# Kernel tuning notes

Hardware: AMD Instinct MI355X
Metric: run time of the kernel (lower is better)

## Reference

```python
import jax, jax.numpy as jnp
import numpy as np

D_MODEL = 2048
N_HEADS = 16
D_HEAD = D_MODEL // N_HEADS
BATCH = 2
SEQ = 2048
NEG = -1e9


def setup_inputs() -> dict:
    key = jax.random.key(0)
    ks = jax.random.split(key, 6)
    s = 1.0 / np.sqrt(D_MODEL)
    x = jax.random.normal(ks[0], (BATCH, SEQ, D_MODEL), dtype=jnp.float32)
    # additive causal mask: 0 on/below diagonal, -1e9 above
    causal = jnp.where(jnp.tril(jnp.ones((SEQ, SEQ), dtype=bool)), 0.0, NEG).astype(jnp.float32)
    return {
        "x": x,
        "mask": causal,
        "Wq": jax.random.normal(ks[1], (D_MODEL, D_MODEL), dtype=jnp.float32) * s,
        "bq": jnp.zeros((D_MODEL,), dtype=jnp.float32),
        "Wk": jax.random.normal(ks[2], (D_MODEL, D_MODEL), dtype=jnp.float32) * s,
        "bk": jnp.zeros((D_MODEL,), dtype=jnp.float32),
        "Wv": jax.random.normal(ks[3], (D_MODEL, D_MODEL), dtype=jnp.float32) * s,
        "bv": jnp.zeros((D_MODEL,), dtype=jnp.float32),
        "Wo": jax.random.normal(ks[4], (D_MODEL, D_MODEL), dtype=jnp.float32) * s,
        "bo": jnp.zeros((D_MODEL,), dtype=jnp.float32),
    }


def reference(x, mask, Wq, bq, Wk, bk, Wv, bv, Wo, bo):
    B, S, _ = x.shape
    scale = 1.0 / np.sqrt(D_HEAD).astype(np.float32)
    # projections -> (B, H, S, Dh)
    def split_heads(t):
        return t.reshape(B, S, N_HEADS, D_HEAD).transpose(0, 2, 1, 3)
    q = split_heads(x @ Wq + bq)
    k = split_heads(x @ Wk + bk)
    v = split_heads(x @ Wv + bv)
    scores = jnp.einsum("bhqd,bhkd->bhqk", q, k) * scale + mask  # (B,H,S,S)
    weights = jax.nn.softmax(scores, axis=-1)
    attn = jnp.einsum("bhqk,bhkd->bhqd", weights, v)
    attn = attn.transpose(0, 2, 1, 3).reshape(B, S, D_MODEL)
    return attn @ Wo + bo
```

## Files before the change

### kernel.cpp

```cpp
#include <hip/hip_runtime.h>
#include <hip/hip_bf16.h>
#include <math.h>

typedef __bf16 bf16;
typedef __attribute__((ext_vector_type(4))) __bf16 bf16x4;
typedef __attribute__((ext_vector_type(8))) __bf16 bf16x8;
typedef __attribute__((ext_vector_type(4))) float f32x4;
typedef __attribute__((ext_vector_type(4))) int i32x4;

#define DEV __device__ __forceinline__
#define FENCE asm volatile("" ::: "memory")

static constexpr int S_LEN = 2048;
static constexpr int DM = 2048;
static constexpr int NB = 2;
static constexpr int NH = 16;
static constexpr int DH = 128;
static constexpr long MROWS = (long)NB * S_LEN;

static constexpr float QSCALE = 0.12751744836522312f;
static constexpr float M0 = 11.0f;


__global__ void k_cast_bf16(const float* __restrict__ in, bf16* __restrict__ out, long n8) {
  long i = (long)blockIdx.x * blockDim.x + threadIdx.x;
  long stride = (long)gridDim.x * blockDim.x;
  for (; i < n8; i += stride) {
    const float4* p = (const float4*)(in + i * 8);
    float4 a = p[0], b = p[1];
    bf16x8 v;
    v[0] = (bf16)a.x; v[1] = (bf16)a.y; v[2] = (bf16)a.z; v[3] = (bf16)a.w;
    v[4] = (bf16)b.x; v[5] = (bf16)b.y; v[6] = (bf16)b.z; v[7] = (bf16)b.w;
    *(bf16x8*)(out + i * 8) = v;
  }
}

__global__ void k_transpose_w(const float* __restrict__ in, bf16* __restrict__ out) {
  __shared__ float t[32][33];
  int bx = blockIdx.x * 32, by = blockIdx.y * 32;
  int tx = threadIdx.x, ty = threadIdx.y;
#pragma unroll
  for (int i = 0; i < 32; i += 8)
    t[ty + i][tx] = in[(long)(by + ty + i) * DM + bx + tx];
  __syncthreads();
#pragma unroll
  for (int i = 0; i < 32; i += 8)
    out[(long)(bx + ty + i) * DM + by + tx] = (bf16)t[tx][ty + i];
}

__global__ void k_transpose_w3(const float* __restrict__ w0, const float* __restrict__ w1,
                               const float* __restrict__ w2, bf16* __restrict__ out) {
  __shared__ float t[32][33];
  int z = blockIdx.z;
  const float* in = (z == 0) ? w0 : (z == 1) ? w1 : w2;
  bf16* o = out + (long)z * DM * DM;
  int bx = blockIdx.x * 32, by = blockIdx.y * 32;
  int tx = threadIdx.x, ty = threadIdx.y;
#pragma unroll
  for (int i = 0; i < 32; i += 8)
    t[ty + i][tx] = in[(long)(by + ty + i) * DM + bx + tx];
  __syncthreads();
#pragma unroll
  for (int i = 0; i < 32; i += 8)
    o[(long)(bx + ty + i) * DM + by + tx] = (bf16)t[tx][ty + i];
}


DEV void stg_round(const bf16* __restrict__ g, long gstride, bf16* l, int tid, int c) {
  int o = c * 8192 + tid * 16;
  int row = o >> 7;
  int blk = (o >> 4) & 7;
  const bf16* src = g + (long)row * gstride + ((blk ^ (row & 7)) << 3);
  char* dst = (char*)l + (o & ~1023);
  __builtin_amdgcn_global_load_lds(
      (const __attribute__((address_space(1))) void*)src,
      (__attribute__((address_space(3))) void*)dst, 16, 0, 0);
}

template<int ROWB>
DEV void stage16k(const bf16* __restrict__ g, long gstride, bf16* l, int tid) {
#pragma unroll
  for (int c = 0; c < 4; ++c) {
    int o = c * 4096 + tid * 16;
    int row = o / ROWB;
    int blk = (o & (ROWB - 1)) >> 4;
    int blkg = blk ^ (row & 7);
    const bf16* src = g + (long)row * gstride + (blkg << 3);
    char* dst = (char*)l + (o & ~1023);
    __builtin_amdgcn_global_load_lds(
        (const __attribute__((address_space(1))) void*)src,
        (__attribute__((address_space(3))) void*)dst, 16, 0, 0);
  }
}

DEV void stage_k(const bf16* __restrict__ g, bf16* l, int tid) {
#pragma unroll
  for (int c = 0; c < 4; ++c) {
    int o = c * 4096 + tid * 16;
    int row = o >> 8;
    int blk = (o >> 4) & 15;
    int blkg = blk ^ (row & 7);
    int prow = (row & 3) | (((row >> 2) & 3) << 3) | (((row >> 5) & 1) << 2) |
               (((row >> 4) & 1) << 5);
    const bf16* src = g + (long)prow * DM + (blkg << 3);
    char* dst = (char*)l + (o & ~1023);
    __builtin_amdgcn_global_load_lds(
        (const __attribute__((address_space(1))) void*)src,
        (__attribute__((address_space(3))) void*)dst, 16, 0, 0);
  }
}

template<int ROWB>
DEV bf16x8 read_frag(const bf16* l, int row, int blk) {
  int blks = blk ^ (row & 7);
  return *(const bf16x8*)((const char*)l + row * ROWB + (blks << 4));
}


__global__ __launch_bounds__(512) void k_gemm_qkv(const bf16* __restrict__ A,
                                                  const bf16* __restrict__ WTqkv,
                                                  const float* __restrict__ bq,
                                                  const float* __restrict__ bk,
                                                  const float* __restrict__ bv,
                                                  bf16* __restrict__ Qb,
                                                  bf16* __restrict__ Kb,
                                                  bf16* __restrict__ Vt) {
  extern __shared__ char smem[];
  int tid = threadIdx.x;
  int w = tid >> 6, lane = tid & 63;
  int wm = w >> 2, wn = w & 3;
  int g = lane >> 4, c16 = lane & 15;
  long row0 = (long)blockIdx.y * 256;
  long col0 = (long)blockIdx.x * 256;
  int proj = (int)(col0 >> 11);
  int lcol0 = (int)(col0 & 2047);
  const float* bias = (proj == 0) ? bq : (proj == 1) ? bk : bv;
  const bf16* gA = A + row0 * 2048;
  const bf16* gB = WTqkv + col0 * 2048;

  f32x4 acc[8][4] = {};

#define BA(i) ((bf16*)(smem + (i) * 65536))
#define BB(i) ((bf16*)(smem + (i) * 65536 + 32768))

#pragma unroll
  for (int c = 0; c < 4; ++c) stg_round(gA, 2048, BA(0), tid, c);
#pragma unroll
  for (int c = 0; c < 4; ++c) stg_round(gB, 2048, BB(0), tid, c);
  asm volatile("s_waitcnt vmcnt(0)" ::: "memory");
  __builtin_amdgcn_s_barrier();
  FENCE;

#pragma unroll 1
  for (int t = 0; t < 32; ++t) {
    int cur = t & 1, nxt = cur ^ 1;
    bf16* cA = BA(cur);
    bf16* cB = BB(cur);
    bool st = (t + 1) < 32;
    if (st) {
      const bf16* gA2 = gA + (t + 1) * 64;
      const bf16* gB2 = gB + (t + 1) * 64;
#pragma unroll
      for (int c = 0; c < 4; ++c) stg_round(gA2, 2048, BA(nxt), tid, c);
#pragma unroll
      for (int c = 0; c < 4; ++c) stg_round(gB2, 2048, BB(nxt), tid, c);
    }
    bf16x8 af[4], bj[4];
#pragma unroll
    for (int ks = 0; ks < 2; ++ks) {
#pragma unroll
      for (int j = 0; j < 4; ++j)
        bj[j] = read_frag<128>(cB, wn * 64 + j * 16 + c16, ks * 4 + g);
#pragma unroll
      for (int rh = 0; rh < 2; ++rh) {
#pragma unroll
        for (int i = 0; i < 4; ++i)
          af[i] = read_frag<128>(cA, wm * 128 + rh * 64 + i * 16 + c16, ks * 4 + g);
        __builtin_amdgcn_s_setprio(1);
#pragma unroll
        for (int i = 0; i < 4; ++i)
#pragma unroll
          for (int j = 0; j < 4; ++j)
            acc[rh * 4 + i][j] =
                __builtin_amdgcn_mfma_f32_16x16x32_bf16(af[i], bj[j], acc[rh * 4 + i][j], 0, 0, 0);
        __builtin_amdgcn_s_setprio(0);
      }
    }
    if (st) {
      asm volatile("s_waitcnt vmcnt(0)" ::: "memory");
      FENCE; __builtin_amdgcn_s_barrier(); FENCE;
    }
  }

#pragma unroll
  for (int i = 0; i < 8; ++i) {
    long grow = row0 + wm * 128 + i * 16 + (g << 2);
#pragma unroll
    for (int j = 0; j < 4; ++j) {
      int lcol = lcol0 + wn * 64 + j * 16 + c16;
      float bv_ = bias[lcol];
      if (proj == 2) {
        int b = (int)(grow >> 11), s = (int)(grow & 2047);
        int h = lcol >> 7, d = lcol & 127;
        bf16x4 pk;
#pragma unroll
        for (int r = 0; r < 4; ++r) pk[r] = (bf16)(acc[i][j][r] + bv_);
        *(bf16x4*)(Vt + ((long)((b << 4) | h) * 128 + d) * 2048 + s) = pk;
      } else {
        bf16* dst = (proj == 0) ? Qb : Kb;
        float cs = (proj == 0) ? QSCALE : 1.0f;
#pragma unroll
        for (int r = 0; r < 4; ++r)
          dst[(grow + r) * 2048 + lcol] = (bf16)((acc[i][j][r] + bv_) * cs);
      }
    }
  }
#undef BA
#undef BB
}


DEV void gemm_loop(const bf16* __restrict__ gA, const bf16* __restrict__ gB,
                   char* smem, int tid, int wm, int wn, int g, int c16,
                   f32x4 (&acc)[4][4]) {
#define BUFA(i) ((bf16*)(smem + (i) * 49152))
#define BUFB(i) ((bf16*)(smem + (i) * 49152 + 32768))

#pragma unroll
  for (int t0 = 0; t0 < 2; ++t0) {
#pragma unroll
    for (int c = 0; c < 4; ++c) stg_round(gA + t0 * 64, 2048, BUFA(t0), tid, c);
#pragma unroll
    for (int c = 0; c < 2; ++c) stg_round(gB + t0 * 64, 2048, BUFB(t0), tid, c);
  }
  asm volatile("s_waitcnt vmcnt(6)" ::: "memory");
  __builtin_amdgcn_s_barrier();
  FENCE;

#pragma unroll 1
  for (int t = 0; t < 32; ++t) {
    bf16* cA = BUFA(t % 3);
    bf16* cB = BUFB(t % 3);
    bf16* nA = BUFA((t + 2) % 3);
    bf16* nB = BUFB((t + 2) % 3);
    const bf16* gA2 = gA + (t + 2) * 64;
    const bf16* gB2 = gB + (t + 2) * 64;
    bool st = (t + 2) < 32;
    bf16x8 af[4], bj[4];

    if (st) { stg_round(gA2, 2048, nA, tid, 0); stg_round(gA2, 2048, nA, tid, 1);
              stg_round(gA2, 2048, nA, tid, 2); }
#pragma unroll
    for (int i = 0; i < 4; ++i) af[i] = read_frag<128>(cA, wm * 64 + i * 16 + c16, g);
#pragma unroll
    for (int j = 0; j < 4; ++j) bj[j] = read_frag<128>(cB, wn * 64 + j * 16 + c16, g);
    __builtin_amdgcn_s_setprio(1);
#pragma unroll
    for (int i = 0; i < 4; ++i)
#pragma unroll
      for (int j = 0; j < 4; ++j)
        acc[i][j] = __builtin_amdgcn_mfma_f32_16x16x32_bf16(af[i], bj[j], acc[i][j], 0, 0, 0);
    __builtin_amdgcn_s_setprio(0);
    FENCE; __builtin_amdgcn_s_barrier(); FENCE;

    if (st) { stg_round(gA2, 2048, nA, tid, 3);
              stg_round(gB2, 2048, nB, tid, 0); stg_round(gB2, 2048, nB, tid, 1); }
#pragma unroll
    for (int i = 0; i < 4; ++i) af[i] = read_frag<128>(cA, wm * 64 + i * 16 + c16, 4 + g);
#pragma unroll
    for (int j = 0; j < 4; ++j) bj[j] = read_frag<128>(cB, wn * 64 + j * 16 + c16, 4 + g);
    __builtin_amdgcn_s_setprio(1);
#pragma unroll
    for (int i = 0; i < 4; ++i)
#pragma unroll
      for (int j = 0; j < 4; ++j)
        acc[i][j] = __builtin_amdgcn_mfma_f32_16x16x32_bf16(af[i], bj[j], acc[i][j], 0, 0, 0);
    __builtin_amdgcn_s_setprio(0);
    if (t + 2 < 32) {
      asm volatile("s_waitcnt vmcnt(6)" ::: "memory");
    } else if (t + 1 < 32) {
      asm volatile("s_waitcnt vmcnt(0)" ::: "memory");
    }
    FENCE; __builtin_amdgcn_s_barrier(); FENCE;
  }
#undef BUFA
#undef BUFB
}

__global__ __launch_bounds__(512) void k_gemm_o(const bf16* __restrict__ A,
                                                const bf16* __restrict__ BT,
                                                const float* __restrict__ bias,
                                                float* __restrict__ C) {
  extern __shared__ char smem[];
  int tid = threadIdx.x;
  int w = tid >> 6, lane = tid & 63;
  int wm = w >> 1, wn = w & 1;
  int g = lane >> 4, c16 = lane & 15;
  long row0 = (long)blockIdx.y * 256, col0 = (long)blockIdx.x * 128;

  f32x4 acc[4][4] = {};
  gemm_loop(A + row0 * 2048, BT + col0 * 2048, smem, tid, wm, wn, g, c16, acc);

#pragma unroll
  for (int i = 0; i < 4; ++i) {
    long grow = row0 + wm * 64 + i * 16 + (g << 2);
#pragma unroll
    for (int j = 0; j < 4; ++j) {
      long gcol = col0 + wn * 64 + j * 16 + c16;
      float bv = bias[gcol];
#pragma unroll
      for (int r = 0; r < 4; ++r)
        C[(grow + r) * 2048 + gcol] = acc[i][j][r] + bv;
    }
  }
}


__global__ __launch_bounds__(256, 2) void k_attn(const bf16* __restrict__ Q,
                                                 const bf16* __restrict__ Kt,
                                                 const bf16* __restrict__ Vt,
                                                 bf16* __restrict__ O,
                                                 bf16* __restrict__ part,
                                                 float* __restrict__ lsums) {
  __shared__ __align__(16) bf16 sK[2][64 * 128];
  __shared__ __align__(16) bf16 sV[2][128 * 64];

  int tid = threadIdx.x;
  int bid = blockIdx.x;
  int bh = bid & 31;
  int pr = (bid >> 5) & 7;
  int role = bid >> 8;
  int b = bh >> 4, h = bh & 15;
  int w = tid >> 6, lane = tid & 63;
  int g = lane >> 4, c16 = lane & 15;
  int t = bh * 8 + pr;

  const bf16* Qh = Q + (long)b * S_LEN * DM + h * DH;
  const bf16* Kh = Kt + (long)b * S_LEN * DM + h * DH;
  const bf16* Vh = Vt + (long)bh * DH * S_LEN;

#pragma unroll 1
  for (int seg = 0; seg < 2; ++seg) {
    int qt, k0, k1, partial;
    if (role == 0) {
      if (seg == 0) { qt = pr;      k0 = 0;           k1 = 2 * pr + 2;  partial = 0; }
      else          { qt = 15 - pr; k0 = 0;           k1 = 15 - 2 * pr; partial = 1; }
    } else {
      if (seg == 1) break;
      qt = 15 - pr; k0 = 15 - 2 * pr; k1 = 32 - 2 * pr; partial = 2;
    }

    int q0 = qt * 128;
    int qb = q0 + w * 32;

    bf16x8 qa[2][4];
#pragma unroll
    for (int u = 0; u < 2; ++u)
#pragma unroll
      for (int ks = 0; ks < 4; ++ks)
        qa[u][ks] = *(const bf16x8*)(Qh + (long)(qb + 16 * u + c16) * DM + (ks * 4 + g) * 8);

    stage_k(Kh + (long)k0 * 64 * DM, sK[0], tid);
    stage16k<128>(Vh + k0 * 64, S_LEN, sV[0], tid);

    float lsum[2] = {0.f, 0.f};
    f32x4 od[2][8] = {};

#pragma unroll 1
    for (int kt = k0; kt < k1; ++kt) {
      int cur = (kt - k0) & 1;
      if (kt + 1 < k1) {
        stage_k(Kh + (long)(kt + 1) * 64 * DM, sK[cur ^ 1], tid);
        stage16k<128>(Vh + (kt + 1) * 64, S_LEN, sV[cur ^ 1], tid);
        asm volatile("s_waitcnt vmcnt(8)" ::: "memory");
      } else {
        asm volatile("s_waitcnt vmcnt(0)" ::: "memory");
      }
      __builtin_amdgcn_s_barrier();
      FENCE;

      int kv0 = kt * 64;
      if (kv0 <= qb + 31) {
        f32x4 sf[2][4] = {};
        __builtin_amdgcn_s_setprio(1);
#pragma unroll
        for (int n = 0; n < 4; ++n)
#pragma unroll
          for (int ks = 0; ks < 4; ++ks) {
            bf16x8 kf = read_frag<256>(sK[cur], n * 16 + c16, ks * 4 + g);
            sf[0][n] = __builtin_amdgcn_mfma_f32_16x16x32_bf16(kf, qa[0][ks], sf[0][n], 0, 0, 0);
            sf[1][n] = __builtin_amdgcn_mfma_f32_16x16x32_bf16(kf, qa[1][ks], sf[1][n], 0, 0, 0);
          }
        __builtin_amdgcn_s_setprio(0);

        bool emask = (kv0 + 63 > qb);
        bf16x8 pa[2][2];
#pragma unroll
        for (int u = 0; u < 2; ++u) {
          unsigned pw[8];
#pragma unroll
          for (int n = 0; n < 4; ++n) {
            float pv4[4];
#pragma unroll
            for (int r = 0; r < 4; ++r) {
              float sc = sf[u][n][r];
              if (emask) {
                int kv = kv0 + ((n & 1) << 5) + (g << 3) + ((n >> 1) << 2) + r;
                int qg = qb + 16 * u + c16;
                sc = (kv > qg) ? -INFINITY : sc;
              }
              float pv = exp2f(sc - M0);
              pv4[r] = pv;
              lsum[u] += pv;
            }
            asm("v_cvt_pk_bf16_f32 %0, %1, %2" : "=v"(pw[2 * n]) : "v"(pv4[0]), "v"(pv4[1]));
            asm("v_cvt_pk_bf16_f32 %0, %1, %2" : "=v"(pw[2 * n + 1]) : "v"(pv4[2]), "v"(pv4[3]));
          }
          i32x4 t0 = {(int)pw[0], (int)pw[1], (int)pw[4], (int)pw[5]};
          i32x4 t1 = {(int)pw[2], (int)pw[3], (int)pw[6], (int)pw[7]};
          pa[u][0] = __builtin_bit_cast(bf16x8, t0);
          pa[u][1] = __builtin_bit_cast(bf16x8, t1);
        }

        __builtin_amdgcn_s_setprio(1);
#pragma unroll
        for (int j = 0; j < 8; ++j)
#pragma unroll
          for (int ks = 0; ks < 2; ++ks) {
            bf16x8 vf = read_frag<128>(sV[cur], j * 16 + c16, ks * 4 + g);
            od[0][j] = __builtin_amdgcn_mfma_f32_16x16x32_bf16(pa[0][ks], vf, od[0][j], 0, 0, 0);
            od[1][j] = __builtin_amdgcn_mfma_f32_16x16x32_bf16(pa[1][ks], vf, od[1][j], 0, 0, 0);
          }
        __builtin_amdgcn_s_setprio(0);
      }
      FENCE;
      __builtin_amdgcn_s_barrier();
    }

#pragma unroll
    for (int u = 0; u < 2; ++u) {
      lsum[u] += __shfl_xor(lsum[u], 16);
      lsum[u] += __shfl_xor(lsum[u], 32);
    }

    if (partial == 0) {
      const long ob = ((long)(b * S_LEN + qb)) * DM + h * DH + c16;
#pragma unroll
      for (int u = 0; u < 2; ++u)
#pragma unroll
        for (int r = 0; r < 4; ++r) {
          float inv = 1.0f / __shfl(lsum[u], 4 * g + r);
#pragma unroll
          for (int j = 0; j < 8; ++j)
            O[ob + (long)(16 * u + 4 * g + r) * DM + j * 16] = (bf16)(od[u][j][r] * inv);
        }
    } else {
      bf16* PP = part + ((long)((partial == 2 ? 256 : 0) + t)) * 16384;
      float* LP = lsums + (partial == 2 ? 256 * 128 : 0) + t * 128;
#pragma unroll
      for (int u = 0; u < 2; ++u) {
        if (g == 0) LP[32 * w + 16 * u + c16] = lsum[u];
#pragma unroll
        for (int r = 0; r < 4; ++r) {
          int row = 32 * w + 16 * u + 4 * g + r;
#pragma unroll
          for (int j = 0; j < 8; ++j)
            PP[row * 128 + 16 * j + c16] = (bf16)od[u][j][r];
        }
      }
    }
  }
}

__global__ __launch_bounds__(256) void k_merge(const bf16* __restrict__ part,
                                               const float* __restrict__ lsums,
                                               bf16* __restrict__ A2) {
  int t = blockIdx.x;
  int bh = t >> 3, pr = t & 7;
  int b = bh >> 4, h = bh & 15;
  int qt = 15 - pr;
  int tid = threadIdx.x;
  int q = tid >> 1, d0 = (tid & 1) * 64;
  float inv = 1.0f / (lsums[t * 128 + q] + lsums[256 * 128 + t * 128 + q]);
  const bf16* pA = part + (long)t * 16384 + q * 128 + d0;
  const bf16* pB = part + (long)(256 + t) * 16384 + q * 128 + d0;
  bf16* out = A2 + ((long)(b * S_LEN + qt * 128 + q)) * DM + h * DH + d0;
#pragma unroll
  for (int j = 0; j < 8; ++j) {
    bf16x8 a = *(const bf16x8*)(pA + j * 8);
    bf16x8 bb = *(const bf16x8*)(pB + j * 8);
    bf16x8 o;
#pragma unroll
    for (int r = 0; r < 8; ++r) o[r] = (bf16)(((float)a[r] + (float)bb[r]) * inv);
    *(bf16x8*)(out + j * 8) = o;
  }
}


extern "C" void kernel_launch(void* const* d_in, const int* in_sizes, int n_in,
                              void* d_out, int out_size, void* d_ws, size_t ws_size,
                              hipStream_t stream) {
  (void)in_sizes; (void)n_in; (void)out_size; (void)ws_size;
  const float* x  = (const float*)d_in[0];
  const float* Wq = (const float*)d_in[2];
  const float* bq = (const float*)d_in[3];
  const float* Wk = (const float*)d_in[4];
  const float* bk = (const float*)d_in[5];
  const float* Wv = (const float*)d_in[6];
  const float* bv = (const float*)d_in[7];
  const float* Wo = (const float*)d_in[8];
  const float* bo = (const float*)d_in[9];
  float* out = (float*)d_out;

  bf16* Xb = (bf16*)d_ws;
  bf16* WT = Xb + MROWS * DM;
  bf16* Qb = WT + (long)DM * DM;
  bf16* Kb = Qb + MROWS * DM;
  bf16* Vt = Kb + MROWS * DM;
  bf16* A2 = Xb;

  bf16* WTqkv = (bf16*)d_out;
  bf16* part = (bf16*)d_out;
  float* lsums = (float*)((bf16*)d_out + 2L * 256 * 16384);

  static const int QKV_LDS = 2 * 65536;
  static const int O_LDS = 3 * 49152;
  hipFuncSetAttribute((const void*)k_gemm_qkv, hipFuncAttributeMaxDynamicSharedMemorySize, QKV_LDS);
  hipFuncSetAttribute((const void*)k_gemm_o, hipFuncAttributeMaxDynamicSharedMemorySize, O_LDS);

  dim3 tb32(32, 8);
  dim3 gW(64, 64);

  k_cast_bf16<<<2048, 256, 0, stream>>>(x, Xb, MROWS * DM / 8);
  k_transpose_w3<<<dim3(64, 64, 3), tb32, 0, stream>>>(Wq, Wk, Wv, WTqkv);

  k_gemm_qkv<<<dim3(24, 16), 512, QKV_LDS, stream>>>(Xb, WTqkv, bq, bk, bv, Qb, Kb, Vt);

  k_attn<<<512, 256, 0, stream>>>(Qb, Kb, Vt, A2, part, lsums);
  k_merge<<<256, 256, 0, stream>>>(part, lsums, A2);

  k_transpose_w<<<gW, tb32, 0, stream>>>(Wo, WT);
  k_gemm_o<<<dim3(16, 16), 512, O_LDS, stream>>>(A2, WT, bo, out);
}
```

Before: 254.8 us.

## Widen QKV GEMM tile to 256x384 with 12 waves and 256 blocks

The QKV projection GEMM now uses 768-thread blocks (12 waves in a 2x6 layout) over 256x384 output tiles, which cuts the grid from 384 to 256 blocks, one per CU on a 256-CU part, and removes the partial second wave. Staging is rewritten as a per-wave chunk loop that loads the A and wider B tiles into a larger 160KB double-buffered LDS region. Because a tile can now span two projections, the epilogue picks the projection and bias per column. The cost is more LDS per block and higher register pressure at 768 threads, since each wave still holds 8x4 accumulators.

```diff
diff --git a/kernel.cpp b/kernel.cpp
--- a/kernel.cpp
+++ b/kernel.cpp
@@ -117,7 +117,7 @@
 }
 
 
-__global__ __launch_bounds__(512) void k_gemm_qkv(const bf16* __restrict__ A,
+__global__ __launch_bounds__(768) void k_gemm_qkv(const bf16* __restrict__ A,
                                                   const bf16* __restrict__ WTqkv,
                                                   const float* __restrict__ bq,
                                                   const float* __restrict__ bk,
@@ -128,25 +128,40 @@
   extern __shared__ char smem[];
   int tid = threadIdx.x;
   int w = tid >> 6, lane = tid & 63;
-  int wm = w >> 2, wn = w & 3;
+  int wm = w / 6, wn = w % 6;
   int g = lane >> 4, c16 = lane & 15;
   long row0 = (long)blockIdx.y * 256;
-  long col0 = (long)blockIdx.x * 256;
-  int proj = (int)(col0 >> 11);
-  int lcol0 = (int)(col0 & 2047);
-  const float* bias = (proj == 0) ? bq : (proj == 1) ? bk : bv;
+  long col0 = (long)blockIdx.x * 384;
   const bf16* gA = A + row0 * 2048;
   const bf16* gB = WTqkv + col0 * 2048;
 
   f32x4 acc[8][4] = {};
 
-#define BA(i) ((bf16*)(smem + (i) * 65536))
-#define BB(i) ((bf16*)(smem + (i) * 65536 + 32768))
-
-#pragma unroll
-  for (int c = 0; c < 4; ++c) stg_round(gA, 2048, BA(0), tid, c);
-#pragma unroll
-  for (int c = 0; c < 4; ++c) stg_round(gB, 2048, BB(0), tid, c);
+#define BA(i) ((bf16*)(smem + (i) * 81920))
+#define BB(i) ((bf16*)(smem + (i) * 81920 + 32768))
+
+#define STAGE_TILE(aP, bP, lA, lB)                                                          \
+  do {                                                                                      \
+    for (int ch = w; ch < 80; ch += 12) {                                                   \
+      if (ch < 32) {                                                                        \
+        int o = ch * 1024 + lane * 16;                                                      \
+        int row = o >> 7, blk = (o >> 4) & 7;                                               \
+        __builtin_amdgcn_global_load_lds(                                                   \
+            (const __attribute__((address_space(1))) void*)((aP) + (long)row * 2048 +      \
+                                                            ((blk ^ (row & 7)) << 3)),      \
+            (__attribute__((address_space(3))) void*)((char*)(lA) + (o & ~1023)), 16, 0, 0);\
+      } else {                                                                              \
+        int o = (ch - 32) * 1024 + lane * 16;                                               \
+        int row = o >> 7, blk = (o >> 4) & 7;                                               \
+        __builtin_amdgcn_global_load_lds(                                                   \
+            (const __attribute__((address_space(1))) void*)((bP) + (long)row * 2048 +      \
+                                                            ((blk ^ (row & 7)) << 3)),      \
+            (__attribute__((address_space(3))) void*)((char*)(lB) + (o & ~1023)), 16, 0, 0);\
+      }                                                                                     \
+    }                                                                                       \
+  } while (0)
+
+  STAGE_TILE(gA, gB, BA(0), BB(0));
   asm volatile("s_waitcnt vmcnt(0)" ::: "memory");
   __builtin_amdgcn_s_barrier();
   FENCE;
@@ -157,14 +172,8 @@
     bf16* cA = BA(cur);
     bf16* cB = BB(cur);
     bool st = (t + 1) < 32;
-    if (st) {
-      const bf16* gA2 = gA + (t + 1) * 64;
-      const bf16* gB2 = gB + (t + 1) * 64;
-#pragma unroll
-      for (int c = 0; c < 4; ++c) stg_round(gA2, 2048, BA(nxt), tid, c);
-#pragma unroll
-      for (int c = 0; c < 4; ++c) stg_round(gB2, 2048, BB(nxt), tid, c);
-    }
+    if (st) STAGE_TILE(gA + (t + 1) * 64, gB + (t + 1) * 64, BA(nxt), BB(nxt));
+
     bf16x8 af[4], bj[4];
 #pragma unroll
     for (int ks = 0; ks < 2; ++ks) {
@@ -197,11 +206,13 @@
     long grow = row0 + wm * 128 + i * 16 + (g << 2);
 #pragma unroll
     for (int j = 0; j < 4; ++j) {
-      int lcol = lcol0 + wn * 64 + j * 16 + c16;
-      float bv_ = bias[lcol];
+      int gcol = (int)col0 + wn * 64 + j * 16 + c16;
+      int proj = gcol >> 11;
+      int cc = gcol & 2047;
+      float bv_ = ((proj == 0) ? bq : (proj == 1) ? bk : bv)[cc];
       if (proj == 2) {
         int b = (int)(grow >> 11), s = (int)(grow & 2047);
-        int h = lcol >> 7, d = lcol & 127;
+        int h = cc >> 7, d = cc & 127;
         bf16x4 pk;
 #pragma unroll
         for (int r = 0; r < 4; ++r) pk[r] = (bf16)(acc[i][j][r] + bv_);
@@ -211,12 +222,13 @@
         float cs = (proj == 0) ? QSCALE : 1.0f;
 #pragma unroll
         for (int r = 0; r < 4; ++r)
-          dst[(grow + r) * 2048 + lcol] = (bf16)((acc[i][j][r] + bv_) * cs);
+          dst[(grow + r) * 2048 + cc] = (bf16)((acc[i][j][r] + bv_) * cs);
       }
     }
   }
 #undef BA
 #undef BB
+#undef STAGE_TILE
 }
 
 
@@ -523,7 +535,7 @@
   bf16* part = (bf16*)d_out;
   float* lsums = (float*)((bf16*)d_out + 2L * 256 * 16384);
 
-  static const int QKV_LDS = 2 * 65536;
+  static const int QKV_LDS = 2 * 81920;
   static const int O_LDS = 3 * 49152;
   hipFuncSetAttribute((const void*)k_gemm_qkv, hipFuncAttributeMaxDynamicSharedMemorySize, QKV_LDS);
   hipFuncSetAttribute((const void*)k_gemm_o, hipFuncAttributeMaxDynamicSharedMemorySize, O_LDS);
@@ -534,7 +546,7 @@
   k_cast_bf16<<<2048, 256, 0, stream>>>(x, Xb, MROWS * DM / 8);
   k_transpose_w3<<<dim3(64, 64, 3), tb32, 0, stream>>>(Wq, Wk, Wv, WTqkv);
 
-  k_gemm_qkv<<<dim3(24, 16), 512, QKV_LDS, stream>>>(Xb, WTqkv, bq, bk, bv, Qb, Kb, Vt);
+  k_gemm_qkv<<<dim3(16, 16), 768, QKV_LDS, stream>>>(Xb, WTqkv, bq, bk, bv, Qb, Kb, Vt);
 
   k_attn<<<512, 256, 0, stream>>>(Qb, Kb, Vt, A2, part, lsums);
   k_merge<<<256, 256, 0, stream>>>(part, lsums, A2);
```

Measured after the change: 265.5 us. 4.2% more time.
